# Kernel optimization log

Measured on AMD Instinct MI355X. Metric: run time of the kernel, lower is better.

The kernel has to match this reference:

```python
import jax, jax.numpy as jnp
import numpy as np

N, L, H, D = 4, 1024, 8, 64

def setup_inputs() -> dict:
    key = jax.random.key(0)
    ks = jax.random.split(key, 6)
    names = ["q_real", "q_imag", "k_real", "k_imag", "v_real", "v_imag"]
    return {n: jax.random.normal(k, (N, L, H, D), dtype=jnp.float32) for n, k in zip(names, ks)}


def reference(q_real, q_imag, k_real, k_imag, v_real, v_imag):
    d = q_real.shape[-1]
    scale = 1.0 / np.sqrt(d).astype(np.float32)
    # complex QK^T: (ar+i*ai)(br+i*bi) -> 4 real einsums, scores shape (N,H,L,S)
    s_real = (jnp.einsum('nlhd,nshd->nhls', q_real, k_real)
              - jnp.einsum('nlhd,nshd->nhls', q_imag, k_imag))
    s_imag = (jnp.einsum('nlhd,nshd->nhls', q_real, k_imag)
              + jnp.einsum('nlhd,nshd->nhls', q_imag, k_real))
    # complex softmax = independent softmax on real and imag parts
    w_real = jax.nn.softmax(scale * s_real, axis=-1)
    w_imag = jax.nn.softmax(scale * s_imag, axis=-1)
    # complex_dropout on complex input is identity (original code drops nothing)
    # complex AV
    u_real = (jnp.einsum('nhls,nshd->nlhd', w_real, v_real)
              - jnp.einsum('nhls,nshd->nlhd', w_imag, v_imag))
    u_imag = (jnp.einsum('nhls,nshd->nlhd', w_real, v_imag)
              + jnp.einsum('nhls,nshd->nlhd', w_imag, v_real))
    # attn_weights.permute(0,2,1,3).mean(dim=-2): (N,H,L,S)->(N,L,H,S), mean over H -> (N,L,S)
    a_real = w_real.mean(axis=1)
    a_imag = w_imag.mean(axis=1)
    return (u_real, u_imag, a_real, a_imag)
```

## Files before the change

kernel.cpp:

```cpp
#include <hip/hip_runtime.h>

#define N_ 4
#define L_ 1024
#define H_ 8
#define D_ 64

typedef _Float16 f16x8 __attribute__((ext_vector_type(8)));
typedef float f32x4 __attribute__((ext_vector_type(4)));

#define MFMA(A, B, C) __builtin_amdgcn_mfma_f32_16x16x32_f16(A, B, C, 0, 0, 0)

__device__ __forceinline__ ushort f2h(float x) {
    union { _Float16 h; ushort u; } c;
    c.h = (_Float16)x;
    return c.u;
}
__device__ __forceinline__ f16x8 ld8(const ushort* p) {
    return *(const f16x8*)p;
}
__device__ __forceinline__ f16x8 negf(f16x8 a) {
    uint4 u = __builtin_bit_cast(uint4, a);
    u.x ^= 0x80008000u; u.y ^= 0x80008000u; u.z ^= 0x80008000u; u.w ^= 0x80008000u;
    return __builtin_bit_cast(f16x8, u);
}
__device__ __forceinline__ f16x8 cvt8s(const float* p, float s) {
    float4 a = *(const float4*)p;
    float4 b = *(const float4*)(p + 4);
    union { f16x8 v; _Float16 e[8]; } u;
    u.e[0] = (_Float16)(a.x * s); u.e[1] = (_Float16)(a.y * s);
    u.e[2] = (_Float16)(a.z * s); u.e[3] = (_Float16)(a.w * s);
    u.e[4] = (_Float16)(b.x * s); u.e[5] = (_Float16)(b.y * s);
    u.e[6] = (_Float16)(b.z * s); u.e[7] = (_Float16)(b.w * s);
    return u.v;
}
#define SCQ 0.18033688011112f
__device__ __forceinline__ f16x8 cvt8(const float* p) { return cvt8s(p, SCQ); }

__device__ __forceinline__ void gl_lds16(const ushort* g, ushort* l) {
    __builtin_amdgcn_global_load_lds(
        (const __attribute__((address_space(1))) unsigned int*)g,
        (__attribute__((address_space(3))) unsigned int*)l, 16, 0, 0);
}

__global__ void cvt_k(const float* __restrict__ k_r, const float* __restrict__ k_i,
                      ushort* __restrict__ dst) {
    int gid = blockIdx.x * 256 + threadIdx.x;
    int aid = gid >> 19;
    int idx = (gid & 0x7FFFF) << 2;
    int d  = idx & 63;
    int l  = (idx >> 6) & 1023;
    int hh = (idx >> 16) & 7;
    int n  = idx >> 19;
    const float* src = aid ? k_i : k_r;
    const float4 v = *(const float4*)(src + (((long)n * 1024 + l) * 8 + hh) * 64 + d);
    ushort4 o = make_ushort4(f2h(v.x), f2h(v.y), f2h(v.z), f2h(v.w));
    *(ushort4*)(dst + ((long)aid << 21) + idx) = o;
}

__global__ void cvt_v(const float* __restrict__ vr, const float* __restrict__ vi,
                      ushort* __restrict__ dst) {
    __shared__ ushort t[64][72];
    int bid = blockIdx.x;
    int aid = bid >> 9;
    int b   = bid & 511;
    int s0  = (b & 15) << 6;
    int hh  = (b >> 4) & 7;
    int n   = b >> 7;
    const float* src = aid ? vi : vr;
    int tid = threadIdx.x;
    int r  = tid >> 4;
    int cq = (tid & 15) << 2;
#pragma unroll
    for (int it = 0; it < 4; ++it) {
        int s = s0 + it * 16 + r;
        const float4 v = *(const float4*)(src + (((long)n * 1024 + s) * 8 + hh) * 64 + cq);
        t[it * 16 + r][cq + 0] = f2h(v.x);
        t[it * 16 + r][cq + 1] = f2h(v.y);
        t[it * 16 + r][cq + 2] = f2h(v.z);
        t[it * 16 + r][cq + 3] = f2h(v.w);
    }
    __syncthreads();
#pragma unroll
    for (int it = 0; it < 4; ++it) {
        int dd = it * 16 + r;
        ushort4 o;
        o.x = t[cq + 0][dd]; o.y = t[cq + 1][dd]; o.z = t[cq + 2][dd]; o.w = t[cq + 3][dd];
        *(ushort4*)(dst + ((long)aid << 21) + (((long)n * 8 + hh) * 64 + dd) * 1024 + s0 + cq) = o;
    }
}

#define BFLY(x)                                                             \
    x += __shfl_xor(x, 1); x += __shfl_xor(x, 2);                           \
    x += __shfl_xor(x, 4); x += __shfl_xor(x, 8);


__launch_bounds__(512, 4)
__global__ void attn_u(const float* __restrict__ qr_g, const float* __restrict__ qi_g,
                       const ushort* __restrict__ ws, float* __restrict__ rdbuf,
                       float* __restrict__ out) {
    __shared__ ushort stgK[2][2][32][64];
    __shared__ ushort stgV[2][2][64][32];
    __shared__ ushort wtl[8][16][32];

    const int tid  = threadIdx.x;
    const int lane = tid & 63;
    const int wv   = tid >> 6;
    const int p    = wv >> 2;
    const int lsub = wv & 3;
    const int col  = lane & 15;
    const int g    = lane >> 4;

    const int id = blockIdx.x;
    const int x  = id & 7;
    const int j  = id >> 3;
    const int nh = x * 4 + (j >> 4);
    const int n  = nh >> 3;
    const int h  = nh & 7;
    const int l0 = (j & 15) * 64 + lsub * 16;

    const ushort* Kr = ws + ((long)nh << 16);
    const ushort* Ki = ws + (1l << 21) + ((long)nh << 16);
    const ushort* Vr = ws + (2l << 21) + ((long)nh << 16);
    const ushort* Vi = ws + (3l << 21) + ((long)nh << 16);

    const long qg = (((long)n * 1024 + l0 + col) * 8 + h) * 64 + g * 8;
    const float sgn = p ? SCQ : -SCQ;
    const f16x8 qr0 = cvt8(qr_g + qg), qr1 = cvt8(qr_g + qg + 32);
    const f16x8 qx0 = cvt8s(qi_g + qg, sgn), qx1 = cvt8s(qi_g + qg + 32, sgn);

    const int krow = lsub * 8 + (lane >> 3);
    const int kbs  = ((lane & 7) ^ (krow & 7)) * 8;
    const int vrow = lsub * 16 + (lane >> 2);
    const int vbs  = ((lane & 3) ^ (vrow & 3)) * 8;
    const ushort* Kst = p ? Ki : Kr;
    const ushort* Vst = p ? Vi : Vr;

    float ds[4] = {0.f, 0.f, 0.f, 0.f};
    f32x4 uA[4], uB[4];
#pragma unroll
    for (int db = 0; db < 4; ++db) {
        uA[db] = (f32x4){0.f, 0.f, 0.f, 0.f};
        uB[db] = (f32x4){0.f, 0.f, 0.f, 0.f};
    }

    const int kx  = (g ^ (col & 7)) * 8;
    const int kx2 = ((g + 4) ^ (col & 7)) * 8;
    const int vx  = (g ^ (col & 3)) * 8;

#define STAGE(buf, cc)                                                       \
    do {                                                                     \
        gl_lds16(Kst + (long)((cc) * 32 + krow) * 64 + kbs,                  \
                 &stgK[buf][p][lsub * 8][0]);                                \
        gl_lds16(Vst + (long)vrow * 1024 + (cc) * 32 + vbs,                  \
                 &stgV[buf][p][lsub * 16][0]);                               \
    } while (0)

    STAGE(0, 0);
    __syncthreads();

    for (int cc = 0; cc < 32; ++cc) {
        const int buf = cc & 1;
        if (cc < 31) STAGE(buf ^ 1, cc + 1);

#pragma unroll
        for (int sb = 0; sb < 2; ++sb) {
            const int row = sb * 16 + col;
            f16x8 ka0 = ld8(&stgK[buf][p][row][kx]);
            f16x8 ka1 = ld8(&stgK[buf][p][row][kx2]);
            f16x8 kb0 = ld8(&stgK[buf][p ^ 1][row][kx]);
            f16x8 kb1 = ld8(&stgK[buf][p ^ 1][row][kx2]);
            f32x4 a0 = (f32x4){0.f, 0.f, 0.f, 0.f};
            a0 = MFMA(qr0, ka0, a0); a0 = MFMA(qr1, ka1, a0);
            a0 = MFMA(qx0, kb0, a0); a0 = MFMA(qx1, kb1, a0);
#pragma unroll
            for (int r = 0; r < 4; ++r) {
                const float wf = exp2f(a0[r]);
                ds[r] += wf;
                const int l = 4 * g + r;
                const int scol = sb * 16 + col;
                const int us = l * 32 + (((scol >> 3) ^ (l & 3)) << 3) + (scol & 7);
                (&wtl[wv][0][0])[us] = f2h(wf);
            }
        }

        f16x8 w0 = ld8(&wtl[wv][col][vx]);
#pragma unroll
        for (int db = 0; db < 4; ++db) {
            const int row = db * 16 + col;
            f16x8 vr0 = ld8(&stgV[buf][0][row][vx]);
            f16x8 vi0 = ld8(&stgV[buf][1][row][vx]);
            uA[db] = MFMA(w0, vr0, uA[db]);
            uB[db] = MFMA(w0, vi0, uB[db]);
        }

        __syncthreads();
    }

    BFLY(ds[0]) BFLY(ds[1]) BFLY(ds[2]) BFLY(ds[3])

    float rd[4];
#pragma unroll
    for (int r = 0; r < 4; ++r) rd[r] = 1.f / ds[r];

    if (col == 0) {
#pragma unroll
        for (int r = 0; r < 4; ++r)
            rdbuf[p * 32768 + nh * 1024 + l0 + 4 * g + r] = rd[r];
    }

#pragma unroll
    for (int db = 0; db < 4; ++db) {
#pragma unroll
        for (int r = 0; r < 4; ++r) {
            uA[db][r] *= rd[r];
            uB[db][r] *= rd[r];
        }
    }

    float* cb = (float*)&stgK[0][0][0][0];
    const int ci = (lsub * 64 + lane) * 16;
    if (p == 1) {
#pragma unroll
        for (int db = 0; db < 4; ++db) *(f32x4*)&cb[ci + db * 4] = uB[db];
    }
    __syncthreads();
    f32x4 oR[4];
    if (p == 0) {
#pragma unroll
        for (int db = 0; db < 4; ++db) oR[db] = uA[db] - *(f32x4*)&cb[ci + db * 4];
    }
    __syncthreads();
    if (p == 1) {
#pragma unroll
        for (int db = 0; db < 4; ++db) *(f32x4*)&cb[ci + db * 4] = uA[db];
    }
    __syncthreads();

    if (p == 0) {
        const long OFF_UI = 2097152;
#pragma unroll
        for (int db = 0; db < 4; ++db) {
            f32x4 oI = uB[db] + *(f32x4*)&cb[ci + db * 4];
#pragma unroll
            for (int r = 0; r < 4; ++r) {
                const int l = l0 + 4 * g + r;
                const int d = db * 16 + col;
                const long base = (((long)n * L_ + l) * H_ + h) * D_ + d;
                out[base] = oR[db][r];
                out[OFF_UI + base] = oI[r];
            }
        }
    }
#undef STAGE
}

__launch_bounds__(256, 4)
__global__ void kern_a(const float* __restrict__ qr_g, const float* __restrict__ qi_g,
                       const ushort* __restrict__ ws, const float* __restrict__ rdbuf,
                       float* __restrict__ out) {
    __shared__ ushort stgK[2][2][64][64];
    __shared__ float lrd[8][2][64];

    const int tid  = threadIdx.x;
    const int lane = tid & 63;
    const int wv   = tid >> 6;
    const int col  = lane & 15;
    const int g    = lane >> 4;

    const int id  = blockIdx.x;
    const int x   = id & 7;
    const int q   = id >> 3;
    const int n   = x >> 1;
    const int idx = (x & 1) * 128 + q;
    const int lt0 = (idx >> 4) * 64;
    const int sc  = idx & 15;
    const int l0  = lt0 + wv * 16;

    const ushort* KrB = ws + ((long)(n * 8) << 16);
    const ushort* KiB = ws + (1l << 21) + ((long)(n * 8) << 16);

#pragma unroll
    for (int i = 0; i < 4; ++i) {
        const int t = i * 256 + tid;
        (&lrd[0][0][0])[t] =
            rdbuf[((t >> 6) & 1) * 32768 + (n * 8 + (t >> 7)) * 1024 + lt0 + (t & 63)];
    }

    const int sp   = wv >> 1;
    const int kbs  = ((lane & 7) ^ (lane >> 3)) * 8;

#define STAGEA(buf, hh)                                                      \
    do {                                                                     \
        const ushort* Kp = (sp ? KiB : KrB) + ((long)(hh) << 16);            \
        _Pragma("unroll")                                                    \
        for (int i = 0; i < 4; ++i) {                                        \
            const int krow = (wv & 1) * 32 + i * 8 + (lane >> 3);            \
            gl_lds16(Kp + (long)(sc * 64 + krow) * 64 + kbs,                 \
                     &stgK[buf][sp][(wv & 1) * 32 + i * 8][0]);              \
        }                                                                    \
    } while (0)

    f32x4 aR[4], aI[4];
#pragma unroll
    for (int i = 0; i < 4; ++i) {
        aR[i] = (f32x4){0.f, 0.f, 0.f, 0.f};
        aI[i] = (f32x4){0.f, 0.f, 0.f, 0.f};
    }

    const int kx  = (g ^ (col & 7)) * 8;
    const int kx2 = ((g + 4) ^ (col & 7)) * 8;

    STAGEA(0, 0);
    __syncthreads();

    for (int h = 0; h < 8; ++h) {
        const int buf = h & 1;
        if (h < 7) STAGEA(buf ^ 1, h + 1);

        const long qg = (((long)n * 1024 + l0 + col) * 8 + h) * 64 + g * 8;
        const f16x8 qr0 = cvt8(qr_g + qg), qr1 = cvt8(qr_g + qg + 32);
        const f16x8 qi0 = cvt8(qi_g + qg), qi1 = cvt8(qi_g + qg + 32);
        const f16x8 qn0 = negf(qi0), qn1 = negf(qi1);

        float rdR[4], rdI[4];
#pragma unroll
        for (int r = 0; r < 4; ++r) {
            rdR[r] = lrd[h][0][wv * 16 + 4 * g + r];
            rdI[r] = lrd[h][1][wv * 16 + 4 * g + r];
        }

#pragma unroll
        for (int sb = 0; sb < 4; ++sb) {
            const int row = sb * 16 + col;
            f16x8 kr0 = ld8(&stgK[buf][0][row][kx]);
            f16x8 kr1 = ld8(&stgK[buf][0][row][kx2]);
            f16x8 ki0 = ld8(&stgK[buf][1][row][kx]);
            f16x8 ki1 = ld8(&stgK[buf][1][row][kx2]);
            f32x4 a0 = (f32x4){0.f, 0.f, 0.f, 0.f};
            a0 = MFMA(qr0, kr0, a0); a0 = MFMA(qr1, kr1, a0);
            a0 = MFMA(qn0, ki0, a0); a0 = MFMA(qn1, ki1, a0);
            f32x4 a1 = (f32x4){0.f, 0.f, 0.f, 0.f};
            a1 = MFMA(qr0, ki0, a1); a1 = MFMA(qr1, ki1, a1);
            a1 = MFMA(qi0, kr0, a1); a1 = MFMA(qi1, kr1, a1);
#pragma unroll
            for (int r = 0; r < 4; ++r) {
                aR[sb][r] += exp2f(a0[r]) * rdR[r];
                aI[sb][r] += exp2f(a1[r]) * rdI[r];
            }
        }
        __syncthreads();
    }

    const long OFF_AR = 4194304;
    const long OFF_AI = 8388608;
#pragma unroll
    for (int sb = 0; sb < 4; ++sb) {
#pragma unroll
        for (int r = 0; r < 4; ++r) {
            const int l = l0 + 4 * g + r;
            const int s = sc * 64 + sb * 16 + col;
            const long ab = ((long)n * 1024 + l) * 1024 + s;
            out[OFF_AR + ab] = aR[sb][r] * 0.125f;
            out[OFF_AI + ab] = aI[sb][r] * 0.125f;
        }
    }
#undef STAGEA
}

extern "C" void kernel_launch(void* const* d_in, const int* in_sizes, int n_in,
                              void* d_out, int out_size, void* d_ws, size_t ws_size,
                              hipStream_t stream) {
    const float* qr = (const float*)d_in[0];
    const float* qi = (const float*)d_in[1];
    const float* kr = (const float*)d_in[2];
    const float* ki = (const float*)d_in[3];
    const float* vr = (const float*)d_in[4];
    const float* vi = (const float*)d_in[5];
    ushort* ws = (ushort*)d_ws;
    float* rdbuf = (float*)((char*)d_ws + (16ull << 20));
    float* out = (float*)d_out;

    hipLaunchKernelGGL(cvt_k, dim3(4096), dim3(256), 0, stream, kr, ki, ws);
    hipLaunchKernelGGL(cvt_v, dim3(1024), dim3(256), 0, stream, vr, vi, ws + (2l << 21));
    hipLaunchKernelGGL(attn_u, dim3(512), dim3(512), 0, stream, qr, qi, ws, rdbuf, out);
    hipLaunchKernelGGL(kern_a, dim3(1024), dim3(256), 0, stream, qr, qi, ws, rdbuf, out);
}
```

Measured before the change: 116.5 us.

## Keep softmax weights in registers via transposed QK MFMA, drop LDS round-trip

The QK^T MFMA operands are swapped so each lane holds score values along the key dimension. That layout lets the exponentiated weights be packed straight into f16x4 A-operands for 16x16x16 MFMAs on V, so the per-wave LDS transpose buffer and its stores and loads go away. The row sum now reduces with two cross-lane shuffles instead of four full butterflies, and the reciprocals are redistributed with shuffles. The trade-off is twice as many, smaller MFMAs for the AV product and round-toward-zero f16 packing of the weights.

```diff
diff --git a/kernel.cpp b/kernel.cpp
--- a/kernel.cpp
+++ b/kernel.cpp
@@ -6,9 +6,12 @@
 #define D_ 64
 
 typedef _Float16 f16x8 __attribute__((ext_vector_type(8)));
+typedef _Float16 f16x4 __attribute__((ext_vector_type(4)));
+typedef _Float16 f16x2 __attribute__((ext_vector_type(2)));
 typedef float f32x4 __attribute__((ext_vector_type(4)));
 
 #define MFMA(A, B, C) __builtin_amdgcn_mfma_f32_16x16x32_f16(A, B, C, 0, 0, 0)
+#define MFMA16(A, B, C) __builtin_amdgcn_mfma_f32_16x16x16f16(A, B, C, 0, 0, 0)
 
 __device__ __forceinline__ ushort f2h(float x) {
     union { _Float16 h; ushort u; } c;
@@ -17,6 +20,15 @@
 }
 __device__ __forceinline__ f16x8 ld8(const ushort* p) {
     return *(const f16x8*)p;
+}
+__device__ __forceinline__ f16x4 ld4(const ushort* p) {
+    return *(const f16x4*)p;
+}
+__device__ __forceinline__ f16x4 pack4(float a, float b, float c, float d) {
+    union { f16x4 v; f16x2 h[2]; } u;
+    u.h[0] = __builtin_bit_cast(f16x2, __builtin_amdgcn_cvt_pkrtz(a, b));
+    u.h[1] = __builtin_bit_cast(f16x2, __builtin_amdgcn_cvt_pkrtz(c, d));
+    return u.v;
 }
 __device__ __forceinline__ f16x8 negf(f16x8 a) {
     uint4 u = __builtin_bit_cast(uint4, a);
@@ -100,7 +112,6 @@
                        float* __restrict__ out) {
     __shared__ ushort stgK[2][2][32][64];
     __shared__ ushort stgV[2][2][64][32];
-    __shared__ ushort wtl[8][16][32];
 
     const int tid  = threadIdx.x;
     const int lane = tid & 63;
@@ -135,7 +146,7 @@
     const ushort* Kst = p ? Ki : Kr;
     const ushort* Vst = p ? Vi : Vr;
 
-    float ds[4] = {0.f, 0.f, 0.f, 0.f};
+    float dsum = 0.f;
     f32x4 uA[4], uB[4];
 #pragma unroll
     for (int db = 0; db < 4; ++db) {
@@ -145,7 +156,8 @@
 
     const int kx  = (g ^ (col & 7)) * 8;
     const int kx2 = ((g + 4) ^ (col & 7)) * 8;
-    const int vx  = (g ^ (col & 3)) * 8;
+    const int vo0 = (((g >> 1) ^ (col & 3)) * 8) + (g & 1) * 4;
+    const int vo1 = ((((g >> 1) + 2) ^ (col & 3)) * 8) + (g & 1) * 4;
 
 #define STAGE(buf, cc)                                                       \
     do {                                                                     \
@@ -162,6 +174,7 @@
         const int buf = cc & 1;
         if (cc < 31) STAGE(buf ^ 1, cc + 1);
 
+        f16x4 pw0, pw1;
 #pragma unroll
         for (int sb = 0; sb < 2; ++sb) {
             const int row = sb * 16 + col;
@@ -170,50 +183,43 @@
             f16x8 kb0 = ld8(&stgK[buf][p ^ 1][row][kx]);
             f16x8 kb1 = ld8(&stgK[buf][p ^ 1][row][kx2]);
             f32x4 a0 = (f32x4){0.f, 0.f, 0.f, 0.f};
-            a0 = MFMA(qr0, ka0, a0); a0 = MFMA(qr1, ka1, a0);
-            a0 = MFMA(qx0, kb0, a0); a0 = MFMA(qx1, kb1, a0);
-#pragma unroll
-            for (int r = 0; r < 4; ++r) {
-                const float wf = exp2f(a0[r]);
-                ds[r] += wf;
-                const int l = 4 * g + r;
-                const int scol = sb * 16 + col;
-                const int us = l * 32 + (((scol >> 3) ^ (l & 3)) << 3) + (scol & 7);
-                (&wtl[wv][0][0])[us] = f2h(wf);
-            }
-        }
-
-        f16x8 w0 = ld8(&wtl[wv][col][vx]);
+            a0 = MFMA(ka0, qr0, a0); a0 = MFMA(ka1, qr1, a0);
+            a0 = MFMA(kb0, qx0, a0); a0 = MFMA(kb1, qx1, a0);
+            const float w0 = exp2f(a0[0]), w1 = exp2f(a0[1]);
+            const float w2 = exp2f(a0[2]), w3 = exp2f(a0[3]);
+            dsum += (w0 + w1) + (w2 + w3);
+            if (sb == 0) pw0 = pack4(w0, w1, w2, w3);
+            else         pw1 = pack4(w0, w1, w2, w3);
+        }
+
 #pragma unroll
         for (int db = 0; db < 4; ++db) {
-            const int row = db * 16 + col;
-            f16x8 vr0 = ld8(&stgV[buf][0][row][vx]);
-            f16x8 vi0 = ld8(&stgV[buf][1][row][vx]);
-            uA[db] = MFMA(w0, vr0, uA[db]);
-            uB[db] = MFMA(w0, vi0, uB[db]);
+            const ushort* vrr = &stgV[buf][0][db * 16 + col][0];
+            const ushort* vri = &stgV[buf][1][db * 16 + col][0];
+            uA[db] = MFMA16(pw0, ld4(vrr + vo0), uA[db]);
+            uA[db] = MFMA16(pw1, ld4(vrr + vo1), uA[db]);
+            uB[db] = MFMA16(pw0, ld4(vri + vo0), uB[db]);
+            uB[db] = MFMA16(pw1, ld4(vri + vo1), uB[db]);
         }
 
         __syncthreads();
     }
 
-    BFLY(ds[0]) BFLY(ds[1]) BFLY(ds[2]) BFLY(ds[3])
-
-    float rd[4];
-#pragma unroll
-    for (int r = 0; r < 4; ++r) rd[r] = 1.f / ds[r];
-
-    if (col == 0) {
-#pragma unroll
-        for (int r = 0; r < 4; ++r)
-            rdbuf[p * 32768 + nh * 1024 + l0 + 4 * g + r] = rd[r];
-    }
+    dsum += __shfl_xor(dsum, 16);
+    dsum += __shfl_xor(dsum, 32);
+    const float rd = 1.f / dsum;
+    if (lane < 16) rdbuf[p * 32768 + nh * 1024 + l0 + col] = rd;
+
+    float rdl[4];
+#pragma unroll
+    for (int r = 0; r < 4; ++r) rdl[r] = __shfl(rd, 4 * g + r);
 
 #pragma unroll
     for (int db = 0; db < 4; ++db) {
 #pragma unroll
         for (int r = 0; r < 4; ++r) {
-            uA[db][r] *= rd[r];
-            uB[db][r] *= rd[r];
+            uA[db][r] *= rdl[r];
+            uB[db][r] *= rdl[r];
         }
     }
 
```

Result: slower. 138.2 us (+18.6%).
